# Kernel optimization log

Hardware: AMD Instinct MI355X
Metric: run time of the kernel (lower is better)

Reference implementation:

```python
import jax, jax.numpy as jnp
import numpy as np

B, IN, HID, OUT = 1024, 512, 128, 64
INP1 = IN + 1  # 513, after prepending ones column


def setup_inputs() -> dict:
    key = jax.random.key(0)
    k1, k2, k3, k4, k5, k6, k7, k8 = jax.random.split(key, 8)
    s1 = 1.0 / np.sqrt(INP1 * INP1)
    s2 = 1.0 / np.sqrt(HID)
    return {
        "img": jax.random.normal(k1, (B, IN), dtype=jnp.float32),
        "tab": jax.random.normal(k2, (B, IN), dtype=jnp.float32),
        "W1": jax.random.uniform(k3, (HID, INP1 * INP1), jnp.float32, -s1, s1),
        "b1": jax.random.uniform(k4, (HID,), jnp.float32, -s1, s1),
        "W2": jax.random.uniform(k5, (HID, HID), jnp.float32, -s2, s2),
        "b2": jax.random.uniform(k6, (HID,), jnp.float32, -s2, s2),
        "W3": jax.random.uniform(k7, (OUT, HID), jnp.float32, -s2, s2),
        "b3": jax.random.uniform(k8, (OUT,), jnp.float32, -s2, s2),
    }


def reference(img, tab, W1, b1, W2, b2, W3, b3):
    ones = jnp.ones((img.shape[0], 1), dtype=img.dtype)
    x = jnp.concatenate([ones, img], axis=1)  # [B, IN+1]
    t = jnp.concatenate([ones, tab], axis=1)  # [B, IN+1]
    # batched outer product, flattened: [B, (IN+1)*(IN+1)]
    fusion = jnp.einsum("bi,bj->bij", x, t).reshape(x.shape[0], -1)
    # dropout is identity in eval mode
    y1 = fusion @ W1.T + b1
    y2 = jnp.tanh(y1 @ W2.T + b2)
    y3 = jax.nn.relu(y2 @ W3.T + b3)
    return y3
```

## Files before the change

kernel.cpp:

```cpp
#include <hip/hip_runtime.h>
#include <hip/hip_bf16.h>

typedef __bf16 bf16x8 __attribute__((ext_vector_type(8)));
typedef float f32x4 __attribute__((ext_vector_type(4)));
typedef float f32x4u __attribute__((ext_vector_type(4), aligned(4)));
typedef unsigned short u16x8 __attribute__((ext_vector_type(8)));

typedef __attribute__((address_space(1))) const unsigned int gu32;
typedef __attribute__((address_space(3))) unsigned int lu32;

#define B_SZ   1024
#define IN_SZ  512
#define HID    128
#define OUT_SZ 64
#define BK     32
#define NKT    16
#define M2     65536

static __device__ __forceinline__ unsigned short f2bf(float f) {
    __hip_bfloat16 h = __float2bfloat16(f);
    return *reinterpret_cast<unsigned short*>(&h);
}

__global__ __launch_bounds__(256) void prep_kernel(
    const float* __restrict__ img, const float* __restrict__ tab,
    unsigned short* __restrict__ tbt, float* __restrict__ xhT,
    float* __restrict__ tc)
{
    const int blk = blockIdx.x;
    for (int j = threadIdx.x; j < 512; j += 256) {
        float v = (j == 0) ? 1.0f : tab[(size_t)blk * IN_SZ + (j - 1)];
        tbt[(size_t)blk * 512 + j] = f2bf(v);
    }
    if (threadIdx.x == 0) tc[blk] = tab[(size_t)blk * IN_SZ + 511];
    if (blk < 513) {
        for (int b = threadIdx.x; b < B_SZ; b += 256)
            xhT[(size_t)blk * B_SZ + b] =
                (blk == 0) ? 1.0f : img[(size_t)b * IN_SZ + (blk - 1)];
    }
}

__global__ __launch_bounds__(256) void prep3_kernel(
    const float* __restrict__ w1, float* __restrict__ wrowT)
{
    const int idx = blockIdx.x * 256 + threadIdx.x;
    if (idx < 513 * 128) {
        const int j = idx >> 7, h = idx & 127;
        wrowT[idx] = w1[((size_t)h * 513 + 512) * 513 + j];
    }
}

__global__ __launch_bounds__(512, 4) void gemm_fused(
    const float* __restrict__ w1, const unsigned short* __restrict__ tbt,
    const float* __restrict__ xhT, const float* __restrict__ tc,
    float* __restrict__ y1acc)
{
    __shared__ unsigned short Als[3][128 * BK];
    __shared__ unsigned short Bls[3][256 * BK];

    const int wgid = (blockIdx.x & 7) * 256 + (blockIdx.x >> 3);
    const int bm = wgid >> 2;
    const int bn = wgid & 3;
    const int n0 = bn * 256;
    const int h0    = bm >> 2;
    const int ibase = (bm & 3) * 128;
    const int tid  = threadIdx.x;
    const int wv   = tid >> 6;
    const int wr   = wv >> 2;
    const int wc   = wv & 3;
    const int lane = tid & 63;
    const int l15  = lane & 15;
    const int kg   = lane >> 4;

    const int ar  = tid >> 2;
    const int acl = (tid & 3) ^ ((ar >> 1) & 3);
    const float* asrcF = w1 + ((size_t)h0 * 513 + ibase + ar) * 513 + acl * 8;

    const unsigned short* bsrc[2];
    int bBase[2];
    #pragma unroll
    for (int q = 0; q < 2; ++q) {
        const int p  = q * 512 + tid;
        const int r  = p >> 2;
        const int cl = (p & 3) ^ ((r >> 1) & 3);
        bsrc[q] = tbt + (size_t)(n0 + r) * 512 + cl * 8;
        bBase[q] = (q * 512 + wv * 64) * 8;
    }

    int aoffs[4], boffs[4];
    #pragma unroll
    for (int ms = 0; ms < 4; ++ms) {
        const int r = wr * 64 + ms * 16 + l15;
        aoffs[ms] = (r * 4 + (kg ^ ((r >> 1) & 3))) * 8;
    }
    #pragma unroll
    for (int ns = 0; ns < 4; ++ns) {
        const int r = wc * 64 + ns * 16 + l15;
        boffs[ns] = (r * 4 + (kg ^ ((r >> 1) & 3))) * 8;
    }

    f32x4 acc[4][4] = {};
    f32x4u rAlo, rAhi;

#define STB(BUF, KT) do {                                                    \
        const int k32_ = (KT) * BK;                                          \
        _Pragma("unroll")                                                    \
        for (int q_ = 0; q_ < 2; ++q_)                                       \
            __builtin_amdgcn_global_load_lds(                                \
                (gu32*)(const void*)(bsrc[q_] + k32_),                       \
                (lu32*)(void*)&Bls[BUF][bBase[q_]], 16, 0, 0);               \
    } while (0)
#define CVW8(DST, LO, HI) do {                                               \
        u16x8 u_;                                                            \
        u_[0] = f2bf((LO)[0]); u_[1] = f2bf((LO)[1]);                        \
        u_[2] = f2bf((LO)[2]); u_[3] = f2bf((LO)[3]);                        \
        u_[4] = f2bf((HI)[0]); u_[5] = f2bf((HI)[1]);                        \
        u_[6] = f2bf((HI)[2]); u_[7] = f2bf((HI)[3]);                        \
        *reinterpret_cast<u16x8*>(DST) = u_;                                 \
    } while (0)

    {
        const f32x4u t0lo = *reinterpret_cast<const f32x4u*>(asrcF);
        const f32x4u t0hi = *reinterpret_cast<const f32x4u*>(asrcF + 4);
        const f32x4u t1lo = *reinterpret_cast<const f32x4u*>(asrcF + 32);
        const f32x4u t1hi = *reinterpret_cast<const f32x4u*>(asrcF + 36);
        CVW8(&Als[0][tid * 8], t0lo, t0hi);
        CVW8(&Als[1][tid * 8], t1lo, t1hi);
        STB(0, 0);
        STB(1, 1);
    }
    __syncthreads();

    #pragma unroll
    for (int kt = 0; kt < NKT; ++kt) {
        const int cur = kt % 3;
        const unsigned short* ab = &Als[cur][0];
        const unsigned short* bb = &Bls[cur][0];

        if (kt >= 1 && kt + 1 < NKT)
            CVW8(&Als[(kt + 1) % 3][tid * 8], rAlo, rAhi);
        if (kt + 2 < NKT) {
            const float* s_ = asrcF + (kt + 2) * 32;
            rAlo = *reinterpret_cast<const f32x4u*>(s_);
            rAhi = *reinterpret_cast<const f32x4u*>(s_ + 4);
        }

        bf16x8 af[4];
        #pragma unroll
        for (int ms = 0; ms < 4; ++ms)
            af[ms] = *reinterpret_cast<const bf16x8*>(&ab[aoffs[ms]]);
        __builtin_amdgcn_s_setprio(1);
        #pragma unroll
        for (int ns = 0; ns < 4; ++ns) {
            const bf16x8 bf = *reinterpret_cast<const bf16x8*>(&bb[boffs[ns]]);
            #pragma unroll
            for (int ms = 0; ms < 4; ++ms)
                acc[ms][ns] = __builtin_amdgcn_mfma_f32_16x16x32_bf16(
                    af[ms], bf, acc[ms][ns], 0, 0, 0);
        }
        __builtin_amdgcn_s_setprio(0);

        if (kt == NKT - 1) break;

        if (kt + 2 >= NKT) asm volatile("s_waitcnt vmcnt(0)" ::: "memory");
        else               asm volatile("s_waitcnt vmcnt(2)" ::: "memory");
        if (kt + 2 < NKT) STB((kt + 2) % 3, kt + 2);
        asm volatile("s_waitcnt lgkmcnt(0)" ::: "memory");
        __builtin_amdgcn_s_barrier();
        __builtin_amdgcn_sched_barrier(0);
    }
#undef STB
#undef CVW8

    const size_t orow = (size_t)h0 * 513;
    float wcv[4][4];
    #pragma unroll
    for (int ms = 0; ms < 4; ++ms)
        #pragma unroll
        for (int v = 0; v < 4; ++v) {
            const int i_ = ibase + wr * 64 + ms * 16 + kg * 4 + v;
            wcv[ms][v] = w1[(orow + i_) * 513 + 512];
        }

    #pragma unroll
    for (int ns = 0; ns < 4; ++ns) {
        const int ncol = n0 + wc * 64 + ns * 16 + l15;
        const float tv = tc[ncol];
        float s0 = 0.f;
        #pragma unroll
        for (int ms = 0; ms < 4; ++ms) {
            const int i_ = ibase + wr * 64 + ms * 16 + kg * 4;
            #pragma unroll
            for (int v = 0; v < 4; ++v)
                s0 += (acc[ms][ns][v] + wcv[ms][v] * tv)
                      * xhT[(size_t)(i_ + v) * B_SZ + ncol];
        }
        s0 += __shfl_xor(s0, 16); s0 += __shfl_xor(s0, 32);
        if (lane < 16) atomicAdd(&y1acc[(size_t)ncol * HID + h0], s0);
    }
}

__global__ __launch_bounds__(128) void tail_kernel(
    const float* __restrict__ img, const float* __restrict__ tab,
    const float* __restrict__ wrowT, float* __restrict__ y1acc)
{
    __shared__ float tls[4][513];
    const int b0 = blockIdx.x * 4;
    const int h  = threadIdx.x;
    #pragma unroll
    for (int q = 0; q < 4; ++q)
        for (int j = h; j < 513; j += 128)
            tls[q][j] = (j == 0) ? 1.0f : tab[(size_t)(b0 + q) * IN_SZ + (j - 1)];
    __syncthreads();
    float a0 = 0.f, a1 = 0.f, a2 = 0.f, a3 = 0.f;
    #pragma unroll 8
    for (int j = 0; j < 513; ++j) {
        const float w = wrowT[j * 128 + h];
        a0 += w * tls[0][j]; a1 += w * tls[1][j];
        a2 += w * tls[2][j]; a3 += w * tls[3][j];
    }
    atomicAdd(&y1acc[(size_t)(b0 + 0) * HID + h], a0 * img[(size_t)(b0 + 0) * IN_SZ + 511]);
    atomicAdd(&y1acc[(size_t)(b0 + 1) * HID + h], a1 * img[(size_t)(b0 + 1) * IN_SZ + 511]);
    atomicAdd(&y1acc[(size_t)(b0 + 2) * HID + h], a2 * img[(size_t)(b0 + 2) * IN_SZ + 511]);
    atomicAdd(&y1acc[(size_t)(b0 + 3) * HID + h], a3 * img[(size_t)(b0 + 3) * IN_SZ + 511]);
}

__global__ __launch_bounds__(512, 4) void gemm_fused_fb(
    const float* __restrict__ w1, const unsigned short* __restrict__ tbt,
    const float* __restrict__ xhT, const float* __restrict__ tc,
    float* __restrict__ y1acc)
{
    __shared__ float          Afs[2][64 * BK];
    __shared__ unsigned short Bls[2][512 * BK];

    const int bm = blockIdx.x >> 1;
    const int bn = blockIdx.x & 1;
    const int m0 = bm * 64;
    const int n0 = bn * 512;
    const int tid  = threadIdx.x;
    const int wv   = tid >> 6;
    const int lane = tid & 63;
    const int l15  = lane & 15;
    const int kg   = lane >> 4;

    const int ar  = tid >> 3;
    const int acl = (tid & 7) ^ (ar & 7);
    const float* asrc = w1 + (size_t)(m0 + ar) * 513 + acl * 4;
    const int aBase = (wv * 64) * 4;

    const unsigned short* bsrc[4];
    int bBase[4];
    #pragma unroll
    for (int q = 0; q < 4; ++q) {
        const int p  = q * 512 + tid;
        const int r  = p >> 2;
        const int cl = (p & 3) ^ ((r >> 1) & 3);
        bsrc[q] = tbt + (size_t)(n0 + r) * 512 + cl * 8;
        bBase[q] = (q * 512 + wv * 64) * 8;
    }

    int aoff0[4], aoff1[4], boffs[4];
    #pragma unroll
    for (int ms = 0; ms < 4; ++ms) {
        const int r = ms * 16 + l15;
        aoff0[ms] = r * 32 + (((kg * 2) + 0) ^ (r & 7)) * 4;
        aoff1[ms] = r * 32 + (((kg * 2) + 1) ^ (r & 7)) * 4;
    }
    #pragma unroll
    for (int ns = 0; ns < 4; ++ns) {
        const int r = wv * 64 + ns * 16 + l15;
        boffs[ns] = ((r << 2) | (kg ^ ((r >> 1) & 3))) * 8;
    }

    f32x4 acc[4][4] = {};

#define STAGE_FB(BUF, KT) do {                                               \
        const int k32_ = (KT) * BK;                                          \
        _Pragma("unroll")                                                    \
        for (int q_ = 0; q_ < 4; ++q_)                                       \
            __builtin_amdgcn_global_load_lds(                                \
                (gu32*)(const void*)(bsrc[q_] + k32_),                       \
                (lu32*)(void*)&Bls[BUF][bBase[q_]], 16, 0, 0);               \
        __builtin_amdgcn_global_load_lds(                                    \
            (gu32*)(const void*)(asrc + k32_),                               \
            (lu32*)(void*)&Afs[BUF][aBase], 16, 0, 0);                       \
    } while (0)

    STAGE_FB(0, 0);
    __syncthreads();

    for (int kt = 0; kt < NKT; ++kt) {
        const int cur = kt & 1;
        if (kt + 1 < NKT) STAGE_FB(cur ^ 1, kt + 1);

        const float*          ab = &Afs[cur][0];
        const unsigned short* bb = &Bls[cur][0];
        bf16x8 bfr[4];
        #pragma unroll
        for (int ns = 0; ns < 4; ++ns)
            bfr[ns] = *reinterpret_cast<const bf16x8*>(&bb[boffs[ns]]);
        #pragma unroll
        for (int ms = 0; ms < 4; ++ms) {
            const f32x4 lo = *reinterpret_cast<const f32x4*>(&ab[aoff0[ms]]);
            const f32x4 hi = *reinterpret_cast<const f32x4*>(&ab[aoff1[ms]]);
            u16x8 u;
            u[0] = f2bf(lo[0]); u[1] = f2bf(lo[1]);
            u[2] = f2bf(lo[2]); u[3] = f2bf(lo[3]);
            u[4] = f2bf(hi[0]); u[5] = f2bf(hi[1]);
            u[6] = f2bf(hi[2]); u[7] = f2bf(hi[3]);
            const bf16x8 af = __builtin_bit_cast(bf16x8, u);
            #pragma unroll
            for (int ns = 0; ns < 4; ++ns)
                acc[ms][ns] = __builtin_amdgcn_mfma_f32_16x16x32_bf16(
                    af, bfr[ns], acc[ms][ns], 0, 0, 0);
        }
        __syncthreads();
    }
#undef STAGE_FB

    const int h0 = m0 / 513;
    const int mb = (h0 + 1) * 513;
    const bool cross = (mb < m0 + 64);

    float wcv[4][4];
    #pragma unroll
    for (int ms = 0; ms < 4; ++ms)
        #pragma unroll
        for (int v = 0; v < 4; ++v)
            wcv[ms][v] = w1[(size_t)(m0 + ms * 16 + kg * 4 + v) * 513 + 512];

    #pragma unroll
    for (int ns = 0; ns < 4; ++ns) {
        const int ncol = n0 + wv * 64 + ns * 16 + l15;
        const float tv = tc[ncol];
        float s0 = 0.f, s1 = 0.f;
        #pragma unroll
        for (int ms = 0; ms < 4; ++ms) {
            #pragma unroll
            for (int v = 0; v < 4; ++v) {
                const int m = m0 + ms * 16 + kg * 4 + v;
                const bool lo = (m < mb);
                const int i = lo ? (m - h0 * 513) : (m - mb);
                const float val = (acc[ms][ns][v] + wcv[ms][v] * tv)
                                  * xhT[(size_t)i * B_SZ + ncol];
                if (lo) s0 += val; else s1 += val;
            }
        }
        s0 += __shfl_xor(s0, 16); s0 += __shfl_xor(s0, 32);
        if (lane < 16) atomicAdd(&y1acc[(size_t)ncol * HID + h0], s0);
        if (cross) {
            s1 += __shfl_xor(s1, 16); s1 += __shfl_xor(s1, 32);
            if (lane < 16 && (h0 + 1) < HID)
                atomicAdd(&y1acc[(size_t)ncol * HID + h0 + 1], s1);
        }
    }
}

__global__ __launch_bounds__(128) void mlp_kernel(
    const float* __restrict__ y1acc, const float* __restrict__ b1,
    const float* __restrict__ W2, const float* __restrict__ b2,
    const float* __restrict__ W3, const float* __restrict__ b3,
    float* __restrict__ out)
{
    __shared__ float y1r[HID];
    __shared__ float y2r[HID];
    const int b = blockIdx.x;
    const int h = threadIdx.x;
    y1r[h] = y1acc[(size_t)b * HID + h] + b1[h];
    __syncthreads();
    float a = b2[h];
    const float* w2r = W2 + (size_t)h * HID;
    #pragma unroll 8
    for (int k = 0; k < HID; ++k) a += w2r[k] * y1r[k];
    y2r[h] = tanhf(a);
    __syncthreads();
    if (h < OUT_SZ) {
        float a3 = b3[h];
        const float* w3r = W3 + (size_t)h * HID;
        #pragma unroll 8
        for (int k = 0; k < HID; ++k) a3 += w3r[k] * y2r[k];
        out[(size_t)b * OUT_SZ + h] = fmaxf(a3, 0.f);
    }
}

extern "C" void kernel_launch(void* const* d_in, const int* in_sizes, int n_in,
                              void* d_out, int out_size, void* d_ws, size_t ws_size,
                              hipStream_t stream) {
    const float* img = (const float*)d_in[0];
    const float* tab = (const float*)d_in[1];
    const float* W1  = (const float*)d_in[2];
    const float* b1  = (const float*)d_in[3];
    const float* W2  = (const float*)d_in[4];
    const float* b2  = (const float*)d_in[5];
    const float* W3  = (const float*)d_in[6];
    const float* b3  = (const float*)d_in[7];
    float* out = (float*)d_out;

    char* ws = (char*)d_ws;
    float*          y1acc = (float*)ws;
    unsigned short* tbt   = (unsigned short*)(ws + 524288);
    float*          xhT   = (float*)(ws + 1572864);
    float*          tc    = (float*)(ws + 3674112);
    float*          wrowT = (float*)(ws + 3678208);
    const size_t need = 3678208ULL + 262656ULL;

    hipMemsetAsync(y1acc, 0, (size_t)B_SZ * HID * sizeof(float), stream);
    prep_kernel<<<dim3(1024), dim3(256), 0, stream>>>(img, tab, tbt, xhT, tc);
    if (ws_size >= need) {
        prep3_kernel<<<dim3(257), dim3(256), 0, stream>>>(W1, wrowT);
        gemm_fused<<<dim3(2048), dim3(512), 0, stream>>>(W1, tbt, xhT, tc, y1acc);
        tail_kernel<<<dim3(256), dim3(128), 0, stream>>>(img, tab, wrowT, y1acc);
    } else {
        gemm_fused_fb<<<dim3(2052), dim3(512), 0, stream>>>(W1, tbt, xhT, tc, y1acc);
    }
    mlp_kernel<<<dim3(1024), dim3(128), 0, stream>>>(y1acc, b1, W2, b2, W3, b3, out);
}
```

Measured before the change: 194.5 us.

## Load B fragments directly from global into registers instead of LDS staging

Removes the LDS triple buffer for the B operand (tbt) and has each lane load its bf16x8 MFMA fragments straight from global memory into a double-buffered register array, prefetching one k-step ahead. This cuts LDS traffic and footprint and drops the vmcnt waits tied to global_load_lds. It lowers the occupancy hint from 4 to 3 blocks per CU to leave room for the extra registers. In exchange, B tiles are no longer shared across waves through LDS, so each of the four wave rows fetches the same B data from global or cache, raising global/L2 traffic. There is also no explicit vmcnt wait before the fragments are used.

```diff
diff --git a/kernel.cpp b/kernel.cpp
--- a/kernel.cpp
+++ b/kernel.cpp
@@ -50,13 +50,12 @@
     }
 }
 
-__global__ __launch_bounds__(512, 4) void gemm_fused(
+__global__ __launch_bounds__(512, 3) void gemm_fused(
     const float* __restrict__ w1, const unsigned short* __restrict__ tbt,
     const float* __restrict__ xhT, const float* __restrict__ tc,
     float* __restrict__ y1acc)
 {
     __shared__ unsigned short Als[3][128 * BK];
-    __shared__ unsigned short Bls[3][256 * BK];
 
     const int wgid = (blockIdx.x & 7) * 256 + (blockIdx.x >> 3);
     const int bm = wgid >> 2;
@@ -76,40 +75,22 @@
     const int acl = (tid & 3) ^ ((ar >> 1) & 3);
     const float* asrcF = w1 + ((size_t)h0 * 513 + ibase + ar) * 513 + acl * 8;
 
-    const unsigned short* bsrc[2];
-    int bBase[2];
-    #pragma unroll
-    for (int q = 0; q < 2; ++q) {
-        const int p  = q * 512 + tid;
-        const int r  = p >> 2;
-        const int cl = (p & 3) ^ ((r >> 1) & 3);
-        bsrc[q] = tbt + (size_t)(n0 + r) * 512 + cl * 8;
-        bBase[q] = (q * 512 + wv * 64) * 8;
-    }
-
-    int aoffs[4], boffs[4];
+    int aoffs[4];
     #pragma unroll
     for (int ms = 0; ms < 4; ++ms) {
         const int r = wr * 64 + ms * 16 + l15;
         aoffs[ms] = (r * 4 + (kg ^ ((r >> 1) & 3))) * 8;
     }
-    #pragma unroll
-    for (int ns = 0; ns < 4; ++ns) {
-        const int r = wc * 64 + ns * 16 + l15;
-        boffs[ns] = (r * 4 + (kg ^ ((r >> 1) & 3))) * 8;
-    }
+
+    const unsigned short* bptr[4];
+    #pragma unroll
+    for (int ns = 0; ns < 4; ++ns)
+        bptr[ns] = tbt + (size_t)(n0 + wc * 64 + ns * 16 + l15) * 512 + kg * 8;
 
     f32x4 acc[4][4] = {};
     f32x4u rAlo, rAhi;
-
-#define STB(BUF, KT) do {                                                    \
-        const int k32_ = (KT) * BK;                                          \
-        _Pragma("unroll")                                                    \
-        for (int q_ = 0; q_ < 2; ++q_)                                       \
-            __builtin_amdgcn_global_load_lds(                                \
-                (gu32*)(const void*)(bsrc[q_] + k32_),                       \
-                (lu32*)(void*)&Bls[BUF][bBase[q_]], 16, 0, 0);               \
-    } while (0)
+    bf16x8 fB[2][4];
+
 #define CVW8(DST, LO, HI) do {                                               \
         u16x8 u_;                                                            \
         u_[0] = f2bf((LO)[0]); u_[1] = f2bf((LO)[1]);                        \
@@ -126,16 +107,20 @@
         const f32x4u t1hi = *reinterpret_cast<const f32x4u*>(asrcF + 36);
         CVW8(&Als[0][tid * 8], t0lo, t0hi);
         CVW8(&Als[1][tid * 8], t1lo, t1hi);
-        STB(0, 0);
-        STB(1, 1);
-    }
-    __syncthreads();
+        rAlo = *reinterpret_cast<const f32x4u*>(asrcF + 64);
+        rAhi = *reinterpret_cast<const f32x4u*>(asrcF + 68);
+        #pragma unroll
+        for (int ns = 0; ns < 4; ++ns)
+            fB[0][ns] = *reinterpret_cast<const bf16x8*>(bptr[ns]);
+    }
+    asm volatile("s_waitcnt lgkmcnt(0)" ::: "memory");
+    __builtin_amdgcn_s_barrier();
+    __builtin_amdgcn_sched_barrier(0);
 
     #pragma unroll
     for (int kt = 0; kt < NKT; ++kt) {
         const int cur = kt % 3;
         const unsigned short* ab = &Als[cur][0];
-        const unsigned short* bb = &Bls[cur][0];
 
         if (kt >= 1 && kt + 1 < NKT)
             CVW8(&Als[(kt + 1) % 3][tid * 8], rAlo, rAhi);
@@ -145,31 +130,33 @@
             rAhi = *reinterpret_cast<const f32x4u*>(s_ + 4);
         }
 
+        if (kt + 1 < NKT) {
+            #pragma unroll
+            for (int ns = 0; ns < 4; ++ns)
+                fB[(kt + 1) & 1][ns] =
+                    *reinterpret_cast<const bf16x8*>(bptr[ns] + (kt + 1) * 32);
+        }
+
         bf16x8 af[4];
         #pragma unroll
         for (int ms = 0; ms < 4; ++ms)
             af[ms] = *reinterpret_cast<const bf16x8*>(&ab[aoffs[ms]]);
+
         __builtin_amdgcn_s_setprio(1);
         #pragma unroll
-        for (int ns = 0; ns < 4; ++ns) {
-            const bf16x8 bf = *reinterpret_cast<const bf16x8*>(&bb[boffs[ns]]);
+        for (int ns = 0; ns < 4; ++ns)
             #pragma unroll
             for (int ms = 0; ms < 4; ++ms)
                 acc[ms][ns] = __builtin_amdgcn_mfma_f32_16x16x32_bf16(
-                    af[ms], bf, acc[ms][ns], 0, 0, 0);
-        }
+                    af[ms], fB[kt & 1][ns], acc[ms][ns], 0, 0, 0);
         __builtin_amdgcn_s_setprio(0);
 
-        if (kt == NKT - 1) break;
-
-        if (kt + 2 >= NKT) asm volatile("s_waitcnt vmcnt(0)" ::: "memory");
-        else               asm volatile("s_waitcnt vmcnt(2)" ::: "memory");
-        if (kt + 2 < NKT) STB((kt + 2) % 3, kt + 2);
-        asm volatile("s_waitcnt lgkmcnt(0)" ::: "memory");
-        __builtin_amdgcn_s_barrier();
-        __builtin_amdgcn_sched_barrier(0);
-    }
-#undef STB
+        if (kt < NKT - 1) {
+            asm volatile("s_waitcnt lgkmcnt(0)" ::: "memory");
+            __builtin_amdgcn_s_barrier();
+            __builtin_amdgcn_sched_barrier(0);
+        }
+    }
 #undef CVW8
 
     const size_t orow = (size_t)h0 * 513;
```

Result: slower. 254.0 us (+30.6%).
